# Optimization experiments

Hardware: AMD Instinct MI355X
Metric: run time of the kernel (lower is better)

The kernel has to match this reference:

```python
import jax, jax.numpy as jnp
import numpy as np

H = 16        # num_heads
LN_EPS = 1e-6

def _ln(x, w, b):
    mu = x.mean(-1, keepdims=True)
    var = ((x - mu) ** 2).mean(-1, keepdims=True)
    return (x - mu) * jax.lax.rsqrt(var + LN_EPS) * w + b

def setup_inputs():
    key = jax.random.key(0)
    ks = jax.random.split(key, 6)
    B, L, S, D = 2, 8192, 512, 1024
    std = 0.02
    return {
        "q_in": jax.random.normal(ks[0], (B, L, D), jnp.float32),
        "kv_in": jax.random.normal(ks[1], (B, S, D), jnp.float32),
        "qn_w": jnp.ones((D,), jnp.float32),
        "qn_b": jnp.zeros((D,), jnp.float32),
        "kvn_w": jnp.ones((D,), jnp.float32),
        "kvn_b": jnp.zeros((D,), jnp.float32),
        "Wq": jax.random.normal(ks[2], (D, D), jnp.float32) * std,
        "Wk": jax.random.normal(ks[3], (D, D), jnp.float32) * std,
        "Wv": jax.random.normal(ks[4], (D, D), jnp.float32) * std,
        "Wo": jax.random.normal(ks[5], (D, D), jnp.float32) * std,
        "bo": jnp.zeros((D,), jnp.float32),
        "gate": jnp.ones((1,), jnp.float32),
    }

def reference(q_in, kv_in, qn_w, qn_b, kvn_w, kvn_b, Wq, Wk, Wv, Wo, bo, gate):
    b, l, hid = q_in.shape
    s = kv_in.shape[1]
    d = hid // H
    scale = d ** -0.5
    q_x = _ln(q_in, qn_w, qn_b)
    kv_x = _ln(kv_in, kvn_w, kvn_b)
    # torch Linear: y = x @ W.T  (weights stored [out, in])
    q = (q_x @ Wq.T).reshape(b, l, H, d).transpose(0, 2, 1, 3)   # [b,H,l,d]
    k = (kv_x @ Wk.T).reshape(b, s, H, d).transpose(0, 2, 1, 3)  # [b,H,s,d]
    v = (kv_x @ Wv.T).reshape(b, s, H, d).transpose(0, 2, 1, 3)  # [b,H,s,d]
    logits = jnp.einsum('bhld,bhsd->bhls', q, k) * scale
    attn = jax.nn.softmax(logits, axis=-1)                       # [b,H,l,s]
    # no-grad diagnostics
    attn_d = jax.lax.stop_gradient(attn).astype(jnp.float32)
    ent_per_head = -(attn_d * jnp.log(attn_d + 1e-9)).sum(-1).mean(axis=(0, 2))  # [H]
    mean_entropy = ent_per_head.mean()
    head_entropy_std = ent_per_head.std()  # population std (unbiased=False)
    top_k = min(4, s)
    top_mass = jax.lax.top_k(attn_d, top_k)[0].sum(-1).mean()
    out = jnp.einsum('bhls,bhsd->bhld', attn, v)
    out = out.transpose(0, 2, 1, 3).reshape(b, l, hid)
    out = (out @ Wo.T + bo) * gate  # dropout=0 -> identity; gate broadcasts
    return (out, mean_entropy, head_entropy_std, top_mass, gate[0])
```

## Files before the change

kernel.cpp:

```cpp
#include <hip/hip_runtime.h>
#include <stdint.h>
#include <stddef.h>


typedef __attribute__((ext_vector_type(8))) short bf16x8;
typedef __attribute__((ext_vector_type(4))) float f32x4;
typedef __attribute__((ext_vector_type(16))) float f32x16;
typedef __attribute__((ext_vector_type(2))) unsigned int u32x2;

#define MFMA(a, b, c)   __builtin_amdgcn_mfma_f32_16x16x32_bf16((a), (b), (c), 0, 0, 0)
#define MFMA32(a, b, c) __builtin_amdgcn_mfma_f32_32x32x16_bf16((a), (b), (c), 0, 0, 0)
#define MED3(a, b, c)   __builtin_amdgcn_fmed3f((a), (b), (c))
#define SBAR()  __builtin_amdgcn_s_barrier()
#define SCHED0() __builtin_amdgcn_sched_barrier(0)

__device__ __forceinline__ float bf2f(unsigned short u) {
  union { unsigned int ui; float f; } cv; cv.ui = ((unsigned int)u) << 16; return cv.f;
}
__device__ __forceinline__ unsigned short f2bf(float f) {
  union { float f; unsigned int ui; } cv; cv.f = f;
  unsigned int u = cv.ui;
  u = u + 0x7fffu + ((u >> 16) & 1u);
  return (unsigned short)(u >> 16);
}
__device__ __forceinline__ unsigned int pk2(float a, float b) {
  union { float f; unsigned int u; } ua, ub; ua.f = a; ub.f = b;
  return __builtin_amdgcn_perm(ub.u, ua.u, 0x07060302u);
}
__device__ __forceinline__ float ex2(float x) {
#if __has_builtin(__builtin_amdgcn_exp2f)
  return __builtin_amdgcn_exp2f(x);
#else
  float r; asm("v_exp_f32 %0, %1" : "=v"(r) : "v"(x)); return r;
#endif
}
__device__ __forceinline__ void pl32swap(unsigned int& a, unsigned int& b) {
#if __has_builtin(__builtin_amdgcn_permlane32_swap)
  u32x2 r = __builtin_amdgcn_permlane32_swap(a, b, false, false);
  a = r[0]; b = r[1];
#else
  asm volatile("v_permlane32_swap_b32 %0, %1" : "+v"(a), "+v"(b));
#endif
}
__device__ __forceinline__ bool is_fp32(const unsigned int* probe) {
  return probe[0] == 0x3F800000u;
}
__device__ __forceinline__ void gl2lds(const unsigned short* g, unsigned short* l) {
  __builtin_amdgcn_global_load_lds(
      (const __attribute__((address_space(1))) void*)(uintptr_t)g,
      (__attribute__((address_space(3))) void*)(unsigned int)(uintptr_t)l,
      16, 0, 0);
}

__device__ __forceinline__ size_t qf_addr(int qg, int d) {
  int b = qg >> 13, q = qg & 8191, h = d >> 6, dd = d & 63;
  int lane = (q & 31) | (((dd >> 3) & 1) << 5);
  return ((((size_t)(b * 16 + h) * 256 + (q >> 5)) * 4 + (dd >> 4)) * 64 + lane) * 8 + (dd & 7);
}
__device__ __forceinline__ size_t kf_addr(int r, int d) {
  int b = r >> 9, s = r & 511, h = d >> 6, dd = d & 63;
  int lane = (s & 31) | (((dd >> 3) & 1) << 5);
  return ((((size_t)(b * 16 + h) * 16 + (s >> 5)) * 4 + (dd >> 4)) * 64 + lane) * 8 + (dd & 7);
}
__device__ __forceinline__ size_t vf_addr(int r, int d) {
  int b = r >> 9, s = r & 511, h = d >> 6, dd = d & 63;
  int lane = (dd & 31) | (((s >> 3) & 1) << 5);
  return (((((size_t)(b * 16 + h) * 16 + (s >> 5)) * 2 + (dd >> 5)) * 2 + ((s >> 4) & 1)) * 64 + lane) * 8 + (s & 7);
}

__device__ __forceinline__ void ln_row_impl(
    bool f32, const void* __restrict__ xv, const void* __restrict__ wv,
    const void* __restrict__ bv, unsigned short* __restrict__ y,
    int row, int tid, float* rs, float* rs2)
{
  float v0, v1, v2, v3, w0, w1, w2, w3, b0, b1, b2, b3;
  if (f32) {
    float4 xr = *(const float4*)((const float*)xv + (size_t)row * 1024 + tid * 4);
    v0 = xr.x; v1 = xr.y; v2 = xr.z; v3 = xr.w;
    float4 wr = *(const float4*)((const float*)wv + tid * 4);
    w0 = wr.x; w1 = wr.y; w2 = wr.z; w3 = wr.w;
    float4 br = *(const float4*)((const float*)bv + tid * 4);
    b0 = br.x; b1 = br.y; b2 = br.z; b3 = br.w;
  } else {
    ushort4 xr = *(const ushort4*)((const unsigned short*)xv + (size_t)row * 1024 + tid * 4);
    v0 = bf2f(xr.x); v1 = bf2f(xr.y); v2 = bf2f(xr.z); v3 = bf2f(xr.w);
    ushort4 wr = *(const ushort4*)((const unsigned short*)wv + tid * 4);
    w0 = bf2f(wr.x); w1 = bf2f(wr.y); w2 = bf2f(wr.z); w3 = bf2f(wr.w);
    ushort4 br = *(const ushort4*)((const unsigned short*)bv + tid * 4);
    b0 = bf2f(br.x); b1 = bf2f(br.y); b2 = bf2f(br.z); b3 = bf2f(br.w);
  }
  float s  = v0 + v1 + v2 + v3;
  float s2 = v0*v0 + v1*v1 + v2*v2 + v3*v3;
  #pragma unroll
  for (int off = 32; off > 0; off >>= 1) {
    s  += __shfl_xor(s, off);
    s2 += __shfl_xor(s2, off);
  }
  if ((tid & 63) == 0) { rs[tid >> 6] = s; rs2[tid >> 6] = s2; }
  __syncthreads();
  s  = rs[0] + rs[1] + rs[2] + rs[3];
  s2 = rs2[0] + rs2[1] + rs2[2] + rs2[3];
  const float mean = s * (1.0f / 1024.0f);
  const float var  = s2 * (1.0f / 1024.0f) - mean * mean;
  const float rstd = 1.0f / sqrtf(var + 1e-6f);
  ushort4 o;
  o.x = f2bf((v0 - mean) * rstd * w0 + b0);
  o.y = f2bf((v1 - mean) * rstd * w1 + b1);
  o.z = f2bf((v2 - mean) * rstd * w2 + b2);
  o.w = f2bf((v3 - mean) * rstd * w3 + b3);
  *(ushort4*)(y + (size_t)row * 1024 + tid * 4) = o;
}

__global__ __launch_bounds__(256) void prep_all(
    const unsigned int* __restrict__ probe,
    const void* __restrict__ q_in, const void* __restrict__ qn_w,
    const void* __restrict__ qn_b, unsigned short* __restrict__ qx,
    const void* __restrict__ w0, const void* __restrict__ w1,
    const void* __restrict__ w2, const void* __restrict__ w3,
    unsigned short* __restrict__ wdst,
    const void* __restrict__ kv_in, const void* __restrict__ kvn_w,
    const void* __restrict__ kvn_b, unsigned short* __restrict__ kvx,
    const void* __restrict__ bo, const void* __restrict__ gate,
    unsigned short* __restrict__ bob, unsigned short* __restrict__ gateb,
    float* __restrict__ stats)
{
  __shared__ float rs[4], rs2[4];
  const bool f32 = is_fp32(probe);
  const int bx = blockIdx.x, tid = threadIdx.x;
  if (bx < 16384) {
    ln_row_impl(f32, q_in, qn_w, qn_b, qx, bx, tid, rs, rs2);
    return;
  }
  const int b2 = bx - 16384;
  if (b2 < 4096) {
    const int m = b2 >> 10;
    const void* src = (m == 0) ? w0 : (m == 1) ? w1 : (m == 2) ? w2 : w3;
    unsigned short* d = wdst + (size_t)m * 1048576;
    const int i = (b2 & 1023) * 1024 + tid * 4;
    ushort4 o;
    if (f32) {
      float4 v = *(const float4*)((const float*)src + i);
      o.x = f2bf(v.x); o.y = f2bf(v.y); o.z = f2bf(v.z); o.w = f2bf(v.w);
    } else {
      o = *(const ushort4*)((const unsigned short*)src + i);
    }
    *(ushort4*)(d + i) = o;
  } else if (b2 < 5120) {
    ln_row_impl(f32, kv_in, kvn_w, kvn_b, kvx, b2 - 4096, tid, rs, rs2);
  } else {
    ushort4 o;
    if (f32) {
      float4 v = *(const float4*)((const float*)bo + tid * 4);
      o.x = f2bf(v.x); o.y = f2bf(v.y); o.z = f2bf(v.z); o.w = f2bf(v.w);
    } else {
      o = *(const ushort4*)((const unsigned short*)bo + tid * 4);
    }
    *(ushort4*)(bob + tid * 4) = o;
    if (tid == 0)
      gateb[0] = f32 ? f2bf(((const float*)gate)[0]) : ((const unsigned short*)gate)[0];
    if (tid < 17) stats[tid] = 0.0f;
  }
}

template <int MODE>
__device__ __forceinline__ void gemm_core(
    const unsigned int* __restrict__ probe,
    const unsigned short* __restrict__ A, const unsigned short* __restrict__ B,
    void* __restrict__ Cv, int N, int K, int m0, int n0,
    const unsigned short* __restrict__ bias, const unsigned short* __restrict__ gate,
    unsigned short* As, unsigned short* Bs)
{
  const int tid = threadIdx.x;
  const int wave = tid >> 6, lane = tid & 63, ln = lane & 15, quad = lane >> 4;
  const int wm = (wave >> 1) * 64, wn = (wave & 1) * 64;
  f32x4 acc[4][4] = {};
  for (int k0 = 0; k0 < K; k0 += 64) {
    __syncthreads();
    #pragma unroll
    for (int i = 0; i < 4; i++) {
      int idx = tid + i * 256;
      int r = idx >> 3, ch = (idx & 7) * 8;
      gl2lds(A + (size_t)(m0 + r) * K + k0 + ch, As + r * 64 + ch);
      gl2lds(B + (size_t)(n0 + r) * K + k0 + ch, Bs + r * 64 + ch);
    }
    __syncthreads();
    #pragma unroll
    for (int kk = 0; kk < 64; kk += 32) {
      bf16x8 af[4], bfr[4];
      #pragma unroll
      for (int i = 0; i < 4; i++) {
        af[i]  = *(const bf16x8*)(As + (wm + i * 16 + ln) * 64 + kk + quad * 8);
        bfr[i] = *(const bf16x8*)(Bs + (wn + i * 16 + ln) * 64 + kk + quad * 8);
      }
      #pragma unroll
      for (int mi = 0; mi < 4; mi++)
        #pragma unroll
        for (int ni = 0; ni < 4; ni++)
          acc[mi][ni] = MFMA(af[mi], bfr[ni], acc[mi][ni]);
    }
  }
  #pragma unroll
  for (int mi = 0; mi < 4; mi++) {
    #pragma unroll
    for (int ni = 0; ni < 4; ni++) {
      const int col = n0 + wn + ni * 16 + ln;
      #pragma unroll
      for (int r = 0; r < 4; r++) {
        const int row = m0 + wm + mi * 16 + quad * 4 + r;
        const float val = acc[mi][ni][r];
        if (col < 1024) ((unsigned short*)Cv)[kf_addr(row, col)] = f2bf(val);
        else ((unsigned short*)Cv)[1048576 + vf_addr(row, col - 1024)] = f2bf(val);
      }
    }
  }
}

template <int MODE>
__global__ __launch_bounds__(256, 3) void gemm_nt(
    const unsigned int* __restrict__ probe,
    const unsigned short* __restrict__ A, const unsigned short* __restrict__ B,
    void* __restrict__ Cv, int M, int N, int K,
    const unsigned short* __restrict__ bias, const unsigned short* __restrict__ gate)
{
  __shared__ unsigned short As[128 * 64];
  __shared__ unsigned short Bs[128 * 64];
  const int nbx = gridDim.x;
  const int nwg = nbx * gridDim.y;
  const int cpx = nwg >> 3;
  const int flat = blockIdx.y * nbx + blockIdx.x;
  const int swz = (flat & 7) * cpx + (flat >> 3);
  const int n0 = (swz % nbx) * 128;
  const int m0 = (swz / nbx) * 128;
  gemm_core<MODE>(probe, A, B, Cv, N, K, m0, n0, bias, gate, As, Bs);
}

#define STG256(mat, row0, base, h, kt) {                                      \
    _Pragma("unroll")                                                         \
    for (int i_ = 0; i_ < 2; i_++) {                                          \
      int rl_ = (h) * 128 + i_ * 64 + (tid >> 3);                             \
      int cb_ = (tid & 7) ^ (((rl_ >> 2) & 1) << 1);                          \
      gl2lds(mat + (size_t)((row0) + rl_) * K + (kt) * 64 + cb_ * 8,          \
             lds + (base) + rl_ * 64 + (tid & 7) * 8);                        \
    } }
#define RDA256(abase, MH, KK) {                                               \
    _Pragma("unroll")                                                         \
    for (int f_ = 0; f_ < 4; f_++) {                                          \
      int rl_ = wm + (MH) * 64 + f_ * 16 + ln;                                \
      af[f_] = *(const bf16x8*)(lds + (abase) + rl_ * 64 +                    \
                 (((KK) + quad * 8) ^ (((rl_ >> 2) & 1) << 4)));              \
    } }
#define RDB256(bbase, KK) {                                                   \
    _Pragma("unroll")                                                         \
    for (int f_ = 0; f_ < 4; f_++) {                                          \
      int rl_ = wn + f_ * 16 + ln;                                            \
      bf[f_] = *(const bf16x8*)(lds + (bbase) + rl_ * 64 +                    \
                 (((KK) + quad * 8) ^ (((rl_ >> 2) & 1) << 4)));              \
    } }
#define MM16(MH) {                                                            \
    __builtin_amdgcn_s_setprio(1);                                            \
    _Pragma("unroll")                                                         \
    for (int mi_ = 0; mi_ < 4; mi_++)                                         \
      _Pragma("unroll")                                                       \
      for (int ni_ = 0; ni_ < 4; ni_++)                                       \
        acc[(MH) * 4 + mi_][ni_] = MFMA(af[mi_], bf[ni_], acc[(MH)*4+mi_][ni_]); \
    __builtin_amdgcn_s_setprio(0); }
#define VM2() asm volatile("s_waitcnt vmcnt(2)" ::: "memory")

template <int MODE>
__global__ __launch_bounds__(512, 1) void gemm256(
    const unsigned int* __restrict__ probe,
    const unsigned short* __restrict__ A, const unsigned short* __restrict__ Bm,
    void* __restrict__ Cv, int M, int N, int K,
    const unsigned short* __restrict__ bias, const unsigned short* __restrict__ gate)
{
  __shared__ unsigned short lds[65536];
  const int tid = threadIdx.x;
  const int wave = tid >> 6, lane = tid & 63, ln = lane & 15, quad = lane >> 4;
  const int wm = (wave >> 2) * 128, wn = (wave & 3) * 64;

  const int nbx = gridDim.x;
  const int nwg = nbx * gridDim.y;
  const int cpx = nwg >> 3;
  const int flat = blockIdx.y * nbx + blockIdx.x;
  const int swz = (flat & 7) * cpx + (flat >> 3);
  const int n0 = (swz % nbx) * 256;
  const int m0 = (swz / nbx) * 256;

  f32x4 acc[8][4] = {};
  const int NT = K >> 6;

  STG256(Bm, n0, 32768, 0, 0) STG256(Bm, n0, 32768, 1, 0)
  STG256(A,  m0, 0,     0, 0) STG256(A,  m0, 0,     1, 0)
  STG256(Bm, n0, 49152, 0, 1)
  VM2();
  SBAR(); SCHED0();

  for (int t = 0; t < NT; t += 2) {
    bf16x8 af[4], bf[4];
    const int t2 = (t + 2 < NT) ? t + 2 : 0;
    const int t3 = (t + 3 < NT) ? t + 3 : 0;
    RDA256(0, 0, 0) RDB256(32768, 0)
    STG256(Bm, n0, 49152, 1, t + 1)
    SBAR(); SCHED0(); MM16(0) SBAR(); SCHED0();
    RDA256(0, 1, 0)
    STG256(A, m0, 16384, 0, t + 1)
    SBAR(); SCHED0(); MM16(1) SBAR(); SCHED0();
    RDA256(0, 0, 32) RDB256(32768, 32)
    STG256(A, m0, 16384, 1, t + 1)
    SBAR(); SCHED0(); MM16(0) SBAR(); SCHED0();
    RDA256(0, 1, 32)
    STG256(Bm, n0, 32768, 0, t2)
    SBAR(); SCHED0(); MM16(1) VM2(); SBAR(); SCHED0();
    RDA256(16384, 0, 0) RDB256(49152, 0)
    STG256(Bm, n0, 32768, 1, t2)
    SBAR(); SCHED0(); MM16(0) SBAR(); SCHED0();
    RDA256(16384, 1, 0)
    STG256(A, m0, 0, 0, t2)
    SBAR(); SCHED0(); MM16(1) SBAR(); SCHED0();
    RDA256(16384, 0, 32) RDB256(49152, 32)
    STG256(A, m0, 0, 1, t2)
    SBAR(); SCHED0(); MM16(0) SBAR(); SCHED0();
    RDA256(16384, 1, 32)
    STG256(Bm, n0, 49152, 0, t3)
    SBAR(); SCHED0(); MM16(1) VM2(); SBAR(); SCHED0();
  }

  const bool f32o = (MODE == 1) && is_fp32(probe);
  const float g = (MODE == 1) ? bf2f(gate[0]) : 1.0f;
  #pragma unroll
  for (int mf = 0; mf < 8; mf++) {
    #pragma unroll
    for (int nf = 0; nf < 4; nf++) {
      const int col = n0 + wn + nf * 16 + ln;
      const float badd = (MODE == 1) ? bf2f(bias[col]) : 0.0f;
      #pragma unroll
      for (int r = 0; r < 4; r++) {
        const int row = m0 + wm + mf * 16 + quad * 4 + r;
        const float val = (acc[mf][nf][r] + badd) * g;
        if (MODE == 1) {
          if (f32o) ((float*)Cv)[(size_t)row * N + col] = val;
          else ((unsigned short*)Cv)[(size_t)row * N + col] = f2bf(val);
        } else {
          ((unsigned short*)Cv)[qf_addr(row, col)] = f2bf(val * 0.18033688f);
        }
      }
    }
  }
}

#define TRK(T0, T1, T2, T3, L, SQ, IDX) {                                     \
    float x_ = S[IDX];                                                        \
    float o0 = T0, o1 = T1, o2 = T2;                                          \
    T0 = fmaxf(o0, x_); T1 = MED3(o0, o1, x_);                                \
    T2 = MED3(o1, o2, x_); T3 = MED3(o2, T3, x_);                             \
    float p_ = ex2(x_); L += p_; SQ = fmaf(p_, x_, SQ); S[IDX] = p_; }

#define MERGE4(A0, A1, A2, A3, B0, B1, B2, B3) {                              \
    float c0 = fmaxf(A0, B3), c1 = fmaxf(A1, B2);                             \
    float c2 = fmaxf(A2, B1), c3 = fmaxf(A3, B0);                             \
    float d0 = fmaxf(c0, c2), d2 = fminf(c0, c2);                             \
    float d1 = fmaxf(c1, c3), d3 = fminf(c1, c3);                             \
    A0 = fmaxf(d0, d1); A1 = fminf(d0, d1);                                   \
    A2 = fmaxf(d2, d3); A3 = fminf(d2, d3); }

__global__ __launch_bounds__(256, 3) void attn_kernel(
    const unsigned short* __restrict__ Qf, const unsigned short* __restrict__ Kf,
    const unsigned short* __restrict__ Vf, unsigned short* __restrict__ ctx,
    float* __restrict__ stats)
{
  __shared__ float red_e[4], red_t[4];
  const int tid = threadIdx.x;
  const int wave = tid >> 6, lane = tid & 63;
  const int qc = blockIdx.x & 63;
  const int bh = blockIdx.x >> 6;
  const int h = bh & 15, bb = bh >> 4;
  const int qt = qc * 4 + wave;

  const unsigned short* qfb = Qf + ((((size_t)bh * 256 + qt) * 4) * 64 + lane) * 8;
  const bf16x8 bq0 = *(const bf16x8*)(qfb);
  const bf16x8 bq1 = *(const bf16x8*)(qfb + 512);
  const bf16x8 bq2 = *(const bf16x8*)(qfb + 1024);
  const bf16x8 bq3 = *(const bf16x8*)(qfb + 1536);

  const unsigned short* kfb = Kf + ((size_t)bh * 64 * 64 + lane) * 8;
  const unsigned short* vfb = Vf + ((size_t)bh * 64 * 64 + lane) * 8;

  float l0 = 0.f, l1 = 0.f, l2 = 0.f, l3 = 0.f;
  float q0 = 0.f, q1 = 0.f, q2 = 0.f, q3 = 0.f;
  float ta0 = -1e30f, ta1 = -1e30f, ta2 = -1e30f, ta3 = -1e30f;
  float tb0 = -1e30f, tb1 = -1e30f, tb2 = -1e30f, tb3 = -1e30f;
  float tc0 = -1e30f, tc1 = -1e30f, tc2 = -1e30f, tc3 = -1e30f;
  float td0 = -1e30f, td1 = -1e30f, td2 = -1e30f, td3 = -1e30f;
  f32x16 Od0 = {}, Od1 = {};

  bf16x8 kf0 = *(const bf16x8*)(kfb);
  bf16x8 kf1 = *(const bf16x8*)(kfb + 512);
  bf16x8 kf2 = *(const bf16x8*)(kfb + 1024);
  bf16x8 kf3 = *(const bf16x8*)(kfb + 1536);

  for (int ch = 0; ch < 16; ch++) {
    const unsigned short* vp = vfb + (size_t)ch * 2048;
    const bf16x8 v00 = *(const bf16x8*)(vp);
    const bf16x8 v01 = *(const bf16x8*)(vp + 512);
    const bf16x8 v10 = *(const bf16x8*)(vp + 1024);
    const bf16x8 v11 = *(const bf16x8*)(vp + 1536);

    f32x16 S = {};
    __builtin_amdgcn_s_setprio(1);
    S = MFMA32(kf0, bq0, S);
    S = MFMA32(kf1, bq1, S);
    S = MFMA32(kf2, bq2, S);
    S = MFMA32(kf3, bq3, S);
    __builtin_amdgcn_s_setprio(0);

    {
      const unsigned short* kp = kfb + (size_t)(ch + 1) * 2048;
      kf0 = *(const bf16x8*)(kp);
      kf1 = *(const bf16x8*)(kp + 512);
      kf2 = *(const bf16x8*)(kp + 1024);
      kf3 = *(const bf16x8*)(kp + 1536);
    }

    TRK(ta0, ta1, ta2, ta3, l0, q0, 0)  TRK(tb0, tb1, tb2, tb3, l1, q1, 4)
    TRK(tc0, tc1, tc2, tc3, l2, q2, 8)  TRK(td0, td1, td2, td3, l3, q3, 12)
    TRK(ta0, ta1, ta2, ta3, l0, q0, 1)  TRK(tb0, tb1, tb2, tb3, l1, q1, 5)
    TRK(tc0, tc1, tc2, tc3, l2, q2, 9)  TRK(td0, td1, td2, td3, l3, q3, 13)
    TRK(ta0, ta1, ta2, ta3, l0, q0, 2)  TRK(tb0, tb1, tb2, tb3, l1, q1, 6)
    TRK(tc0, tc1, tc2, tc3, l2, q2, 10) TRK(td0, td1, td2, td3, l3, q3, 14)
    TRK(ta0, ta1, ta2, ta3, l0, q0, 3)  TRK(tb0, tb1, tb2, tb3, l1, q1, 7)
    TRK(tc0, tc1, tc2, tc3, l2, q2, 11) TRK(td0, td1, td2, td3, l3, q3, 15)

    unsigned int W0 = pk2(S[0],  S[1]),  W1 = pk2(S[2],  S[3]);
    unsigned int W2 = pk2(S[4],  S[5]),  W3 = pk2(S[6],  S[7]);
    unsigned int W4 = pk2(S[8],  S[9]),  W5 = pk2(S[10], S[11]);
    unsigned int W6 = pk2(S[12], S[13]), W7 = pk2(S[14], S[15]);
    pl32swap(W0, W2); pl32swap(W1, W3);
    pl32swap(W4, W6); pl32swap(W5, W7);
    union { unsigned int u[4]; bf16x8 v; } pb0, pb1;
    pb0.u[0] = W0; pb0.u[1] = W1; pb0.u[2] = W2; pb0.u[3] = W3;
    pb1.u[0] = W4; pb1.u[1] = W5; pb1.u[2] = W6; pb1.u[3] = W7;

    __builtin_amdgcn_s_setprio(1);
    Od0 = MFMA32(v00, pb0.v, Od0);
    Od0 = MFMA32(v01, pb1.v, Od0);
    Od1 = MFMA32(v10, pb0.v, Od1);
    Od1 = MFMA32(v11, pb1.v, Od1);
    __builtin_amdgcn_s_setprio(0);
  }

  MERGE4(ta0, ta1, ta2, ta3, tc0, tc1, tc2, tc3)
  MERGE4(tb0, tb1, tb2, tb3, td0, td1, td2, td3)
  MERGE4(ta0, ta1, ta2, ta3, tb0, tb1, tb2, tb3)
  float lq = (l0 + l1) + (l2 + l3);
  float sq = (q0 + q1) + (q2 + q3);
  lq += __shfl_xor(lq, 32);
  sq += __shfl_xor(sq, 32);
  {
    float o0 = __shfl_xor(ta0, 32), o1 = __shfl_xor(ta1, 32);
    float o2 = __shfl_xor(ta2, 32), o3 = __shfl_xor(ta3, 32);
    MERGE4(ta0, ta1, ta2, ta3, o0, o1, o2, o3)
  }
  const float invl = 1.0f / lq;
  float esum = 0.69314718f * (__log2f(lq) - sq * invl);
  float tsum = (ex2(ta0) + ex2(ta1) + ex2(ta2) + ex2(ta3)) * invl;
  #pragma unroll
  for (int off = 1; off < 64; off <<= 1) {
    esum += __shfl_xor(esum, off);
    tsum += __shfl_xor(tsum, off);
  }
  if (lane == 0) { red_e[wave] = esum * 0.5f; red_t[wave] = tsum * 0.5f; }
  __syncthreads();
  if (tid == 0) {
    atomicAdd(&stats[h],  red_e[0] + red_e[1] + red_e[2] + red_e[3]);
    atomicAdd(&stats[16], red_t[0] + red_t[1] + red_t[2] + red_t[3]);
  }

  const int qrow = lane & 31, hf = lane >> 5;
  unsigned short* cp = ctx + ((size_t)bb * 8192 + (size_t)qt * 32 + qrow) * 1024
                       + h * 64 + hf * 4;
  #pragma unroll
  for (int rg = 0; rg < 4; rg++) {
    ushort4 o;
    o.x = f2bf(Od0[rg * 4 + 0] * invl); o.y = f2bf(Od0[rg * 4 + 1] * invl);
    o.z = f2bf(Od0[rg * 4 + 2] * invl); o.w = f2bf(Od0[rg * 4 + 3] * invl);
    *(ushort4*)(cp + rg * 8) = o;
    o.x = f2bf(Od1[rg * 4 + 0] * invl); o.y = f2bf(Od1[rg * 4 + 1] * invl);
    o.z = f2bf(Od1[rg * 4 + 2] * invl); o.w = f2bf(Od1[rg * 4 + 3] * invl);
    *(ushort4*)(cp + 32 + rg * 8) = o;
  }
}

__global__ void finalize_kernel(const unsigned int* __restrict__ probe,
                                const float* __restrict__ stats,
                                const unsigned short* __restrict__ gateb,
                                void* __restrict__ out)
{
  if (threadIdx.x != 0) return;
  const bool f32 = is_fp32(probe);
  float e[16], s = 0.0f;
  for (int i = 0; i < 16; i++) { e[i] = stats[i] * (1.0f / 16384.0f); s += e[i]; }
  const float mean = s * (1.0f / 16.0f);
  float var = 0.0f;
  for (int i = 0; i < 16; i++) { float d = e[i] - mean; var += d * d; }
  var *= (1.0f / 16.0f);
  const float stdv = sqrtf(var);
  const float tm = stats[16] * (1.0f / 262144.0f);
  const float gv = bf2f(gateb[0]);
  if (f32) {
    float* t = (float*)out + 16777216;
    t[0] = mean; t[1] = stdv; t[2] = tm; t[3] = gv;
  } else {
    unsigned short* t = (unsigned short*)out + 16777216;
    t[0] = f2bf(mean); t[1] = f2bf(stdv); t[2] = f2bf(tm); t[3] = f2bf(gv);
  }
}

extern "C" void kernel_launch(void* const* d_in, const int* in_sizes, int n_in,
                              void* d_out, int out_size, void* d_ws, size_t ws_size,
                              hipStream_t stream)
{
  const void* q_in  = d_in[0];
  const void* kv_in = d_in[1];
  const unsigned int* probe = (const unsigned int*)d_in[2];
  const void* qn_w  = d_in[2];
  const void* qn_b  = d_in[3];
  const void* kvn_w = d_in[4];
  const void* kvn_b = d_in[5];
  const void* Wq    = d_in[6];
  const void* Wk    = d_in[7];
  const void* Wv    = d_in[8];
  const void* Wo    = d_in[9];
  const void* bo    = d_in[10];
  const void* gate  = d_in[11];

  unsigned short* ws    = (unsigned short*)d_ws;
  unsigned short* qx    = ws;
  unsigned short* kvx   = qx + 16777216;
  unsigned short* kfrag = kvx + 1048576;
  unsigned short* vfrag = kfrag + 1048576;
  unsigned short* wcv   = vfrag + 1048576;
  unsigned short* bob   = wcv + 4194304;
  unsigned short* gateb = bob + 1024;
  float* stats = (float*)(gateb + 8);
  unsigned short* qfrag = (unsigned short*)d_out;

  prep_all<<<21505, 256, 0, stream>>>(probe, q_in, qn_w, qn_b, qx,
                                      Wq, Wk, Wv, Wo, wcv,
                                      kv_in, kvn_w, kvn_b, kvx,
                                      bo, gate, bob, gateb, stats);
  gemm_nt<5><<<dim3(16, 8), 256, 0, stream>>>(probe, kvx, wcv + 1048576, kfrag,
                                              1024, 2048, 1024, nullptr, nullptr);
  gemm256<2><<<dim3(4, 64), 512, 0, stream>>>(probe, qx, wcv, qfrag,
                                              16384, 1024, 1024, nullptr, nullptr);
  attn_kernel<<<2048, 256, 0, stream>>>(qfrag, kfrag, vfrag, qx , stats);
  gemm256<1><<<dim3(4, 64), 512, 0, stream>>>(probe, qx, wcv + 3145728, d_out,
                                              16384, 1024, 1024, bob, gateb);
  finalize_kernel<<<1, 64, 0, stream>>>(probe, stats, gateb, d_out);
}
```

Measured before the change: 318.7 us.

## Use plain row-major Q/K and transposed V layouts; fold finalize into output GEMM

Replaces the MFMA-fragment swizzled layouts for Q, K and V with a row-major Q, a per-head row-major K, and a per-head transposed V, and updates the attention kernel's fragment loads to match. It also removes the separate finalize kernel and computes the entropy/top-mass scalars in one thread of the output GEMM. The aim is simpler, more contiguous epilogue stores and one fewer kernel launch. The risks are less coalesced fragment loads in attention and a finalize that reads stats written by the previous kernel with no extra synchronization beyond stream order.

```diff
diff --git a/kernel.cpp b/kernel.cpp
--- a/kernel.cpp
+++ b/kernel.cpp
@@ -50,22 +50,6 @@
       (const __attribute__((address_space(1))) void*)(uintptr_t)g,
       (__attribute__((address_space(3))) void*)(unsigned int)(uintptr_t)l,
       16, 0, 0);
-}
-
-__device__ __forceinline__ size_t qf_addr(int qg, int d) {
-  int b = qg >> 13, q = qg & 8191, h = d >> 6, dd = d & 63;
-  int lane = (q & 31) | (((dd >> 3) & 1) << 5);
-  return ((((size_t)(b * 16 + h) * 256 + (q >> 5)) * 4 + (dd >> 4)) * 64 + lane) * 8 + (dd & 7);
-}
-__device__ __forceinline__ size_t kf_addr(int r, int d) {
-  int b = r >> 9, s = r & 511, h = d >> 6, dd = d & 63;
-  int lane = (s & 31) | (((dd >> 3) & 1) << 5);
-  return ((((size_t)(b * 16 + h) * 16 + (s >> 5)) * 4 + (dd >> 4)) * 64 + lane) * 8 + (dd & 7);
-}
-__device__ __forceinline__ size_t vf_addr(int r, int d) {
-  int b = r >> 9, s = r & 511, h = d >> 6, dd = d & 63;
-  int lane = (dd & 31) | (((s >> 3) & 1) << 5);
-  return (((((size_t)(b * 16 + h) * 16 + (s >> 5)) * 2 + (dd >> 5)) * 2 + ((s >> 4) & 1)) * 64 + lane) * 8 + (s & 7);
 }
 
 __device__ __forceinline__ void ln_row_impl(
@@ -162,14 +146,19 @@
   }
 }
 
-template <int MODE>
-__device__ __forceinline__ void gemm_core(
-    const unsigned int* __restrict__ probe,
+__global__ __launch_bounds__(256, 3) void gemm_kv(
     const unsigned short* __restrict__ A, const unsigned short* __restrict__ B,
-    void* __restrict__ Cv, int N, int K, int m0, int n0,
-    const unsigned short* __restrict__ bias, const unsigned short* __restrict__ gate,
-    unsigned short* As, unsigned short* Bs)
+    unsigned short* __restrict__ Km, int N, int K)
 {
+  __shared__ unsigned short As[128 * 64];
+  __shared__ unsigned short Bs[128 * 64];
+  const int nbx = gridDim.x;
+  const int nwg = nbx * gridDim.y;
+  const int cpx = nwg >> 3;
+  const int flat = blockIdx.y * nbx + blockIdx.x;
+  const int swz = (flat & 7) * cpx + (flat >> 3);
+  const int n0 = (swz % nbx) * 128;
+  const int m0 = (swz / nbx) * 128;
   const int tid = threadIdx.x;
   const int wave = tid >> 6, lane = tid & 63, ln = lane & 15, quad = lane >> 4;
   const int wm = (wave >> 1) * 64, wn = (wave & 1) * 64;
@@ -199,6 +188,7 @@
           acc[mi][ni] = MFMA(af[mi], bfr[ni], acc[mi][ni]);
     }
   }
+  unsigned short* Vt = Km + 1048576;
   #pragma unroll
   for (int mi = 0; mi < 4; mi++) {
     #pragma unroll
@@ -207,31 +197,18 @@
       #pragma unroll
       for (int r = 0; r < 4; r++) {
         const int row = m0 + wm + mi * 16 + quad * 4 + r;
+        const int b = row >> 9, s = row & 511;
         const float val = acc[mi][ni][r];
-        if (col < 1024) ((unsigned short*)Cv)[kf_addr(row, col)] = f2bf(val);
-        else ((unsigned short*)Cv)[1048576 + vf_addr(row, col - 1024)] = f2bf(val);
+        if (col < 1024) {
+          const int h = col >> 6, dd = col & 63;
+          Km[(((size_t)(b * 16 + h) * 512 + s) * 64) + dd] = f2bf(val);
+        } else {
+          const int d2 = col - 1024, h = d2 >> 6, dd = d2 & 63;
+          Vt[((size_t)(b * 16 + h) * 64 + dd) * 512 + s] = f2bf(val);
+        }
       }
     }
   }
-}
-
-template <int MODE>
-__global__ __launch_bounds__(256, 3) void gemm_nt(
-    const unsigned int* __restrict__ probe,
-    const unsigned short* __restrict__ A, const unsigned short* __restrict__ B,
-    void* __restrict__ Cv, int M, int N, int K,
-    const unsigned short* __restrict__ bias, const unsigned short* __restrict__ gate)
-{
-  __shared__ unsigned short As[128 * 64];
-  __shared__ unsigned short Bs[128 * 64];
-  const int nbx = gridDim.x;
-  const int nwg = nbx * gridDim.y;
-  const int cpx = nwg >> 3;
-  const int flat = blockIdx.y * nbx + blockIdx.x;
-  const int swz = (flat & 7) * cpx + (flat >> 3);
-  const int n0 = (swz % nbx) * 128;
-  const int m0 = (swz / nbx) * 128;
-  gemm_core<MODE>(probe, A, B, Cv, N, K, m0, n0, bias, gate, As, Bs);
 }
 
 #define STG256(mat, row0, base, h, kt) {                                      \
@@ -271,7 +248,8 @@
     const unsigned int* __restrict__ probe,
     const unsigned short* __restrict__ A, const unsigned short* __restrict__ Bm,
     void* __restrict__ Cv, int M, int N, int K,
-    const unsigned short* __restrict__ bias, const unsigned short* __restrict__ gate)
+    const unsigned short* __restrict__ bias, const unsigned short* __restrict__ gate,
+    const float* __restrict__ stats)
 {
   __shared__ unsigned short lds[65536];
   const int tid = threadIdx.x;
@@ -341,9 +319,28 @@
           if (f32o) ((float*)Cv)[(size_t)row * N + col] = val;
           else ((unsigned short*)Cv)[(size_t)row * N + col] = f2bf(val);
         } else {
-          ((unsigned short*)Cv)[qf_addr(row, col)] = f2bf(val * 0.18033688f);
+          ((unsigned short*)Cv)[(size_t)row * N + col] = f2bf(val * 0.18033688f);
         }
       }
+    }
+  }
+
+  if (MODE == 1 && flat == 0 && tid == 0) {
+    float e[16], s = 0.0f;
+    for (int i = 0; i < 16; i++) { e[i] = stats[i] * (1.0f / 16384.0f); s += e[i]; }
+    const float mean = s * (1.0f / 16.0f);
+    float var = 0.0f;
+    for (int i = 0; i < 16; i++) { float d = e[i] - mean; var += d * d; }
+    var *= (1.0f / 16.0f);
+    const float stdv = sqrtf(var);
+    const float tm = stats[16] * (1.0f / 262144.0f);
+    const float gv = bf2f(gate[0]);
+    if (f32o) {
+      float* t = (float*)Cv + 16777216;
+      t[0] = mean; t[1] = stdv; t[2] = tm; t[3] = gv;
+    } else {
+      unsigned short* t = (unsigned short*)Cv + 16777216;
+      t[0] = f2bf(mean); t[1] = f2bf(stdv); t[2] = f2bf(tm); t[3] = f2bf(gv);
     }
   }
 }
@@ -364,8 +361,8 @@
     A2 = fmaxf(d2, d3); A3 = fminf(d2, d3); }
 
 __global__ __launch_bounds__(256, 3) void attn_kernel(
-    const unsigned short* __restrict__ Qf, const unsigned short* __restrict__ Kf,
-    const unsigned short* __restrict__ Vf, unsigned short* __restrict__ ctx,
+    const unsigned short* __restrict__ Qm, const unsigned short* __restrict__ Km,
+    const unsigned short* __restrict__ Vt, unsigned short* __restrict__ ctx,
     float* __restrict__ stats)
 {
   __shared__ float red_e[4], red_t[4];
@@ -375,15 +372,17 @@
   const int bh = blockIdx.x >> 6;
   const int h = bh & 15, bb = bh >> 4;
   const int qt = qc * 4 + wave;
-
-  const unsigned short* qfb = Qf + ((((size_t)bh * 256 + qt) * 4) * 64 + lane) * 8;
+  const int rl = lane & 31, hf = lane >> 5;
+
+  const unsigned short* qfb = Qm + ((size_t)bb * 8192 + qt * 32 + rl) * 1024
+                              + h * 64 + hf * 8;
   const bf16x8 bq0 = *(const bf16x8*)(qfb);
-  const bf16x8 bq1 = *(const bf16x8*)(qfb + 512);
-  const bf16x8 bq2 = *(const bf16x8*)(qfb + 1024);
-  const bf16x8 bq3 = *(const bf16x8*)(qfb + 1536);
-
-  const unsigned short* kfb = Kf + ((size_t)bh * 64 * 64 + lane) * 8;
-  const unsigned short* vfb = Vf + ((size_t)bh * 64 * 64 + lane) * 8;
+  const bf16x8 bq1 = *(const bf16x8*)(qfb + 16);
+  const bf16x8 bq2 = *(const bf16x8*)(qfb + 32);
+  const bf16x8 bq3 = *(const bf16x8*)(qfb + 48);
+
+  const unsigned short* kfb = Km + ((size_t)bh * 512 + rl) * 64 + hf * 8;
+  const unsigned short* vfb = Vt + ((size_t)bh * 64 + rl) * 512 + hf * 8;
 
   float l0 = 0.f, l1 = 0.f, l2 = 0.f, l3 = 0.f;
   float q0 = 0.f, q1 = 0.f, q2 = 0.f, q3 = 0.f;
@@ -394,16 +393,16 @@
   f32x16 Od0 = {}, Od1 = {};
 
   bf16x8 kf0 = *(const bf16x8*)(kfb);
-  bf16x8 kf1 = *(const bf16x8*)(kfb + 512);
-  bf16x8 kf2 = *(const bf16x8*)(kfb + 1024);
-  bf16x8 kf3 = *(const bf16x8*)(kfb + 1536);
+  bf16x8 kf1 = *(const bf16x8*)(kfb + 16);
+  bf16x8 kf2 = *(const bf16x8*)(kfb + 32);
+  bf16x8 kf3 = *(const bf16x8*)(kfb + 48);
 
   for (int ch = 0; ch < 16; ch++) {
-    const unsigned short* vp = vfb + (size_t)ch * 2048;
+    const unsigned short* vp = vfb + ch * 32;
     const bf16x8 v00 = *(const bf16x8*)(vp);
-    const bf16x8 v01 = *(const bf16x8*)(vp + 512);
-    const bf16x8 v10 = *(const bf16x8*)(vp + 1024);
-    const bf16x8 v11 = *(const bf16x8*)(vp + 1536);
+    const bf16x8 v01 = *(const bf16x8*)(vp + 16);
+    const bf16x8 v10 = *(const bf16x8*)(vp + 16384);
+    const bf16x8 v11 = *(const bf16x8*)(vp + 16400);
 
     f32x16 S = {};
     __builtin_amdgcn_s_setprio(1);
@@ -416,9 +415,9 @@
     {
       const unsigned short* kp = kfb + (size_t)(ch + 1) * 2048;
       kf0 = *(const bf16x8*)(kp);
-      kf1 = *(const bf16x8*)(kp + 512);
-      kf2 = *(const bf16x8*)(kp + 1024);
-      kf3 = *(const bf16x8*)(kp + 1536);
+      kf1 = *(const bf16x8*)(kp + 16);
+      kf2 = *(const bf16x8*)(kp + 32);
+      kf3 = *(const bf16x8*)(kp + 48);
     }
 
     TRK(ta0, ta1, ta2, ta3, l0, q0, 0)  TRK(tb0, tb1, tb2, tb3, l1, q1, 4)
@@ -475,8 +474,7 @@
     atomicAdd(&stats[16], red_t[0] + red_t[1] + red_t[2] + red_t[3]);
   }
 
-  const int qrow = lane & 31, hf = lane >> 5;
-  unsigned short* cp = ctx + ((size_t)bb * 8192 + (size_t)qt * 32 + qrow) * 1024
+  unsigned short* cp = ctx + ((size_t)bb * 8192 + (size_t)qt * 32 + rl) * 1024
                        + h * 64 + hf * 4;
   #pragma unroll
   for (int rg = 0; rg < 4; rg++) {
@@ -487,31 +485,6 @@
     o.x = f2bf(Od1[rg * 4 + 0] * invl); o.y = f2bf(Od1[rg * 4 + 1] * invl);
     o.z = f2bf(Od1[rg * 4 + 2] * invl); o.w = f2bf(Od1[rg * 4 + 3] * invl);
     *(ushort4*)(cp + 32 + rg * 8) = o;
-  }
-}
-
-__global__ void finalize_kernel(const unsigned int* __restrict__ probe,
-                                const float* __restrict__ stats,
-                                const unsigned short* __restrict__ gateb,
-                                void* __restrict__ out)
-{
-  if (threadIdx.x != 0) return;
-  const bool f32 = is_fp32(probe);
-  float e[16], s = 0.0f;
-  for (int i = 0; i < 16; i++) { e[i] = stats[i] * (1.0f / 16384.0f); s += e[i]; }
-  const float mean = s * (1.0f / 16.0f);
-  float var = 0.0f;
-  for (int i = 0; i < 16; i++) { float d = e[i] - mean; var += d * d; }
-  var *= (1.0f / 16.0f);
-  const float stdv = sqrtf(var);
-  const float tm = stats[16] * (1.0f / 262144.0f);
-  const float gv = bf2f(gateb[0]);
-  if (f32) {
-    float* t = (float*)out + 16777216;
-    t[0] = mean; t[1] = stdv; t[2] = tm; t[3] = gv;
-  } else {
-    unsigned short* t = (unsigned short*)out + 16777216;
-    t[0] = f2bf(mean); t[1] = f2bf(stdv); t[2] = f2bf(tm); t[3] = f2bf(gv);
   }
 }
 
@@ -536,24 +509,24 @@
   unsigned short* ws    = (unsigned short*)d_ws;
   unsigned short* qx    = ws;
   unsigned short* kvx   = qx + 16777216;
-  unsigned short* kfrag = kvx + 1048576;
-  unsigned short* vfrag = kfrag + 1048576;
-  unsigned short* wcv   = vfrag + 1048576;
+  unsigned short* kmat  = kvx + 1048576;
+  unsigned short* vtmat = kmat + 1048576;
+  unsigned short* wcv   = vtmat + 1048576;
   unsigned short* bob   = wcv + 4194304;
   unsigned short* gateb = bob + 1024;
   float* stats = (float*)(gateb + 8);
-  unsigned short* qfrag = (unsigned short*)d_out;
+  unsigned short* qmat = (unsigned short*)d_out;
 
   prep_all<<<21505, 256, 0, stream>>>(probe, q_in, qn_w, qn_b, qx,
                                       Wq, Wk, Wv, Wo, wcv,
                                       kv_in, kvn_w, kvn_b, kvx,
                                       bo, gate, bob, gateb, stats);
-  gemm_nt<5><<<dim3(16, 8), 256, 0, stream>>>(probe, kvx, wcv + 1048576, kfrag,
-                                              1024, 2048, 1024, nullptr, nullptr);
-  gemm256<2><<<dim3(4, 64), 512, 0, stream>>>(probe, qx, wcv, qfrag,
-                                              16384, 1024, 1024, nullptr, nullptr);
-  attn_kernel<<<2048, 256, 0, stream>>>(qfrag, kfrag, vfrag, qx , stats);
+  gemm_kv<<<dim3(16, 8), 256, 0, stream>>>(kvx, wcv + 1048576, kmat, 2048, 1024);
+  gemm256<2><<<dim3(4, 64), 512, 0, stream>>>(probe, qx, wcv, qmat,
+                                              16384, 1024, 1024, nullptr, nullptr,
+                                              nullptr);
+  attn_kernel<<<2048, 256, 0, stream>>>(qmat, kmat, vtmat, qx , stats);
   gemm256<1><<<dim3(4, 64), 512, 0, stream>>>(probe, qx, wcv + 3145728, d_out,
-                                              16384, 1024, 1024, bob, gateb);
-  finalize_kernel<<<1, 64, 0, stream>>>(probe, stats, gateb, d_out);
-}
+                                              16384, 1024, 1024, bob, gateb,
+                                              stats);
+}
```

After: 380.4 us. 19.3% more time.
